# Performance work log

Measured on AMD Instinct MI355X. Metric: run time of the kernel, lower is better.

Reference implementation:

```python
import jax, jax.numpy as jnp
import numpy as np

D = 512      # n_embd
H = 8        # n_head
L = 2        # n_layer (per stack)
T = 2048     # sequence length / block_size
B = 1        # batch
BANDS = (999, 9)  # band_width for [phase, tool] stacks
EPS = 1e-5


def _sinusoidal(n_pos, dim):
    pos = np.arange(n_pos)[:, None].astype(np.float64)
    j = np.arange(dim)[None, :]
    angle = pos / np.power(10000.0, 2 * (j // 2) / dim)
    out = np.zeros((n_pos, dim), np.float32)
    out[:, 0::2] = np.sin(angle[:, 0::2])
    out[:, 1::2] = np.cos(angle[:, 1::2])
    return jnp.asarray(out)


def setup_inputs() -> dict:
    key = jax.random.key(0)
    ks = jax.random.split(key, 8)
    s = 0.02
    rn = lambda k, shp: jax.random.normal(k, shp, jnp.float32) * s
    inp = {
        "x": jax.random.normal(ks[0], (B, T, D), jnp.float32),
        "pos_emb": _sinusoidal(T, D),            # sinusoidal, frozen
        # leading dim 2 = [phase stack, tool stack], then layer dim L
        "ln1_w": jnp.ones((2, L, D)), "ln1_b": jnp.zeros((2, L, D)),
        "ln2_w": jnp.ones((2, L, D)), "ln2_b": jnp.zeros((2, L, D)),
        "Wq": rn(ks[1], (2, L, D, D)), "bq": jnp.zeros((2, L, D)),
        "Wk": rn(ks[2], (2, L, D, D)), "bk": jnp.zeros((2, L, D)),
        "Wv": rn(ks[3], (2, L, D, D)), "bv": jnp.zeros((2, L, D)),
        "Wo": rn(ks[4], (2, L, D, D)), "bo": jnp.zeros((2, L, D)),
        "W1": rn(ks[5], (2, L, D, 2 * D)), "b1": jnp.zeros((2, L, 2 * D)),
        "W2": rn(ks[6], (2, L, 2 * D, D)), "b2": jnp.zeros((2, L, D)),
        "lnf_w": jnp.ones((D,)), "lnf_b": jnp.zeros((D,)),
    }
    return inp


def _ln(x, w, b):
    mu = x.mean(-1, keepdims=True)
    var = ((x - mu) ** 2).mean(-1, keepdims=True)
    return (x - mu) / jnp.sqrt(var + EPS) * w + b


def _attn(x, Wq, bq, Wk, bk, Wv, bv, Wo, bo, bw):
    Bx, Tx, _ = x.shape
    Dh = D // H
    heads = lambda W, b: (x @ W + b).reshape(Bx, Tx, H, Dh).transpose(0, 2, 1, 3)
    q, k, v = heads(Wq, bq), heads(Wk, bk), heads(Wv, bv)
    att = jnp.einsum('bhqd,bhkd->bhqk', q, k) / jnp.sqrt(jnp.float32(Dh))
    i = jnp.arange(Tx)[:, None]
    j = jnp.arange(Tx)[None, :]
    mask = (j <= i) & (j >= i - bw)  # causal band
    att = jnp.where(mask, att, -jnp.inf)
    att = jax.nn.softmax(att, axis=-1)
    y = jnp.einsum('bhqk,bhkd->bhqd', att, v).transpose(0, 2, 1, 3).reshape(Bx, Tx, D)
    return y @ Wo + bo


def reference(x, pos_emb, ln1_w, ln1_b, ln2_w, ln2_b,
              Wq, bq, Wk, bk, Wv, bv, Wo, bo,
              W1, b1, W2, b2, lnf_w, lnf_b):
    Tx = x.shape[1]
    h0 = x + pos_emb[None, :Tx]
    outs = []
    for s in range(2):  # phase stack, tool stack
        bw = BANDS[s]
        h = h0
        for l in range(L):
            h = h + _attn(_ln(h, ln1_w[s, l], ln1_b[s, l]),
                          Wq[s, l], bq[s, l], Wk[s, l], bk[s, l],
                          Wv[s, l], bv[s, l], Wo[s, l], bo[s, l], bw)
            hm = _ln(h, ln2_w[s, l], ln2_b[s, l])
            h = h + (jax.nn.gelu(hm @ W1[s, l] + b1[s, l], approximate=False)
                     @ W2[s, l] + b2[s, l])
        outs.append(_ln(h, lnf_w, lnf_b))
    return (outs[0], outs[1])
```

## Files before the change

kernel.cpp:

```cpp
#include <hip/hip_runtime.h>
#include <stdint.h>

#define T 2048
#define D 512
#define NH 8
#define DH 64
#define L 2

typedef float floatx4 __attribute__((ext_vector_type(4)));
typedef short shortx8 __attribute__((ext_vector_type(8)));
typedef unsigned short u16;
typedef unsigned short u16x4 __attribute__((ext_vector_type(4)));

__device__ __forceinline__ u16 f2bf(float f) {
    union { float f; uint32_t u; } c; c.f = f;
    uint32_t u = c.u;
    u += 0x7fffu + ((u >> 16) & 1u);
    return (u16)(u >> 16);
}

__device__ __forceinline__ float bf2f(u16 v) {
    union { uint32_t u; float f; } c; c.u = ((uint32_t)v) << 16;
    return c.f;
}

__device__ __forceinline__ void load_lds16(const void* g, void* l) {
    __builtin_amdgcn_global_load_lds((const __attribute__((address_space(1))) void*)g,
                                     (__attribute__((address_space(3))) void*)l,
                                     16, 0, 0);
}

struct TransJobs {
    const float* src[6];
    u16* dst[6];
    const float* x;
    const float* pos;
    float* h;
};

__global__ __launch_bounds__(256) void pre_kernel(TransJobs j) {
    __shared__ float tile[32][33];
    int tid = threadIdx.x;
    if (blockIdx.z == 24) {
        int idx = (blockIdx.y * 32 + blockIdx.x) * 256 + tid;
        float4 xv = ((const float4*)j.x)[idx];
        float4 pv = ((const float4*)j.pos)[idx];
        float4 r;
        r.x = xv.x + pv.x; r.y = xv.y + pv.y; r.z = xv.z + pv.z; r.w = xv.w + pv.w;
        ((float4*)j.h)[idx] = r;
        ((float4*)j.h)[idx + (T * D / 4)] = r;
        return;
    }
    int m = blockIdx.z >> 2, slice = blockIdx.z & 3;
    int R = (m == 5) ? 1024 : 512;
    int C = (m == 4) ? 1024 : 512;
    if (blockIdx.x * 32 >= C || blockIdx.y * 32 >= R) return;
    const float* in = j.src[m] + (size_t)slice * R * C;
    u16* out = j.dst[m] + (size_t)slice * R * C;
    int tx = tid & 31, ty = tid >> 5;
    int x = blockIdx.x * 32 + tx;
    int y0 = blockIdx.y * 32;
#pragma unroll
    for (int i = 0; i < 4; i++)
        tile[ty + i * 8][tx] = in[(size_t)(y0 + ty + i * 8) * C + x];
    __syncthreads();
    int ox = y0 + tx;
#pragma unroll
    for (int i = 0; i < 4; i++)
        out[(size_t)(blockIdx.x * 32 + ty + i * 8) * R + ox] = f2bf(tile[tx][ty + i * 8]);
}

__global__ __launch_bounds__(256) void ln_res_kernel(float* __restrict__ h,
                                                     const u16* __restrict__ part,
                                                     const float* __restrict__ w0,
                                                     const float* __restrict__ b0,
                                                     u16* __restrict__ out, int l) {
    int row = blockIdx.x * 4 + (threadIdx.x >> 6);
    int lane = threadIdx.x & 63;
    int s = row >> 11;
    int c0 = lane * 4;
    float* xr = h + (size_t)row * D;
    float4 v0 = *(const float4*)(xr + c0);
    float4 v1 = *(const float4*)(xr + c0 + 256);
    if (part) {
        const u16* p0r = part + (size_t)s * 2 * T * D + (size_t)(row & (T - 1)) * D;
        const u16* p1r = p0r + (size_t)T * D;
        u16x4 a0 = *(const u16x4*)(p0r + c0), a1 = *(const u16x4*)(p0r + c0 + 256);
        u16x4 e0 = *(const u16x4*)(p1r + c0), e1 = *(const u16x4*)(p1r + c0 + 256);
        v0.x += bf2f(a0[0]) + bf2f(e0[0]); v0.y += bf2f(a0[1]) + bf2f(e0[1]);
        v0.z += bf2f(a0[2]) + bf2f(e0[2]); v0.w += bf2f(a0[3]) + bf2f(e0[3]);
        v1.x += bf2f(a1[0]) + bf2f(e1[0]); v1.y += bf2f(a1[1]) + bf2f(e1[1]);
        v1.z += bf2f(a1[2]) + bf2f(e1[2]); v1.w += bf2f(a1[3]) + bf2f(e1[3]);
        *(float4*)(xr + c0) = v0;
        *(float4*)(xr + c0 + 256) = v1;
    }
    float sum = v0.x + v0.y + v0.z + v0.w + v1.x + v1.y + v1.z + v1.w;
    float sq = v0.x*v0.x + v0.y*v0.y + v0.z*v0.z + v0.w*v0.w
             + v1.x*v1.x + v1.y*v1.y + v1.z*v1.z + v1.w*v1.w;
#pragma unroll
    for (int d2 = 1; d2 < 64; d2 <<= 1) { sum += __shfl_xor(sum, d2); sq += __shfl_xor(sq, d2); }
    float mu = sum * (1.0f / D);
    float var = sq * (1.0f / D) - mu * mu;
    float rstd = rsqrtf(var + 1e-5f);
    const float* w = w0 + (size_t)(s * L + l) * D;
    const float* b = b0 + (size_t)(s * L + l) * D;
    u16x4 p0, p1;
#pragma unroll
    for (int jj = 0; jj < 4; jj++) {
        float a = (jj == 0 ? v0.x : jj == 1 ? v0.y : jj == 2 ? v0.z : v0.w);
        p0[jj] = f2bf((a - mu) * rstd * w[c0 + jj] + b[c0 + jj]);
        float c = (jj == 0 ? v1.x : jj == 1 ? v1.y : jj == 2 ? v1.z : v1.w);
        p1[jj] = f2bf((c - mu) * rstd * w[c0 + 256 + jj] + b[c0 + 256 + jj]);
    }
    *(u16x4*)(out + (size_t)row * D + c0) = p0;
    *(u16x4*)(out + (size_t)row * D + c0 + 256) = p1;
}

__global__ __launch_bounds__(256) void lnf_kernel(const float* __restrict__ h,
                                                  const u16* __restrict__ part,
                                                  const float* __restrict__ w,
                                                  const float* __restrict__ b,
                                                  float* __restrict__ out) {
    int row = blockIdx.x * 4 + (threadIdx.x >> 6);
    int lane = threadIdx.x & 63;
    int s = row >> 11;
    int c0 = lane * 4;
    const float* xr = h + (size_t)row * D;
    float4 v0 = *(const float4*)(xr + c0);
    float4 v1 = *(const float4*)(xr + c0 + 256);
    const u16* p0r = part + (size_t)s * 2 * T * D + (size_t)(row & (T - 1)) * D;
    const u16* p1r = p0r + (size_t)T * D;
    u16x4 a0 = *(const u16x4*)(p0r + c0), a1 = *(const u16x4*)(p0r + c0 + 256);
    u16x4 e0 = *(const u16x4*)(p1r + c0), e1 = *(const u16x4*)(p1r + c0 + 256);
    v0.x += bf2f(a0[0]) + bf2f(e0[0]); v0.y += bf2f(a0[1]) + bf2f(e0[1]);
    v0.z += bf2f(a0[2]) + bf2f(e0[2]); v0.w += bf2f(a0[3]) + bf2f(e0[3]);
    v1.x += bf2f(a1[0]) + bf2f(e1[0]); v1.y += bf2f(a1[1]) + bf2f(e1[1]);
    v1.z += bf2f(a1[2]) + bf2f(e1[2]); v1.w += bf2f(a1[3]) + bf2f(e1[3]);
    float sum = v0.x + v0.y + v0.z + v0.w + v1.x + v1.y + v1.z + v1.w;
    float sq = v0.x*v0.x + v0.y*v0.y + v0.z*v0.z + v0.w*v0.w
             + v1.x*v1.x + v1.y*v1.y + v1.z*v1.z + v1.w*v1.w;
#pragma unroll
    for (int d2 = 1; d2 < 64; d2 <<= 1) { sum += __shfl_xor(sum, d2); sq += __shfl_xor(sq, d2); }
    float mu = sum * (1.0f / D);
    float var = sq * (1.0f / D) - mu * mu;
    float rstd = rsqrtf(var + 1e-5f);
    float4 r0, r1;
    r0.x = (v0.x - mu) * rstd * w[c0+0] + b[c0+0];
    r0.y = (v0.y - mu) * rstd * w[c0+1] + b[c0+1];
    r0.z = (v0.z - mu) * rstd * w[c0+2] + b[c0+2];
    r0.w = (v0.w - mu) * rstd * w[c0+3] + b[c0+3];
    r1.x = (v1.x - mu) * rstd * w[c0+256+0] + b[c0+256+0];
    r1.y = (v1.y - mu) * rstd * w[c0+256+1] + b[c0+256+1];
    r1.z = (v1.z - mu) * rstd * w[c0+256+2] + b[c0+256+2];
    r1.w = (v1.w - mu) * rstd * w[c0+256+3] + b[c0+256+3];
    *(float4*)(out + (size_t)row * D + c0) = r0;
    *(float4*)(out + (size_t)row * D + c0 + 256) = r1;
}

struct GemmPtrs {
    const u16* A[6];
    const u16* Bt[6];
    const float* bias[6];
    void* C[6];
};

#define EPI_QKV  0
#define EPI_GELU 1
#define EPI_PART 2

template <int EPI>
__global__ __launch_bounds__(256) void gemm_kernel(GemmPtrs p, int M, int N, int K, int KS) {
    __shared__ __align__(16) u16 lA[2][128 * 32];
    __shared__ __align__(16) u16 lB[2][64 * 32];
    int nchunk = K / KS;
    int pidx = blockIdx.z / nchunk;
    int kc = blockIdx.z % nchunk;
    int koff = kc * KS;
    const u16* A = p.A[pidx];
    const u16* Bt = p.Bt[pidx];
    int m0 = blockIdx.y * 128, n0 = blockIdx.x * 64;
    int tid = threadIdx.x;
    int lane = tid & 63, wave = tid >> 6;
    int wx = wave & 1, wy = wave >> 1;
    int l16 = lane & 15, q4 = lane >> 4;
    const u16* ag = A + (size_t)(m0 + (tid >> 2)) * K + koff + (tid & 3) * 8;
    const u16* bg = Bt + (size_t)(n0 + (tid >> 2)) * K + koff + (tid & 3) * 8;
    size_t rowskip = (size_t)64 * K;
    floatx4 acc[4][2] = {};
    for (int k0 = 0; k0 < KS; k0 += 64) {
        __syncthreads();
#pragma unroll
        for (int kh = 0; kh < 2; kh++) {
            load_lds16(ag + k0 + kh * 32, &lA[kh][tid * 8]);
            load_lds16(ag + rowskip + k0 + kh * 32, &lA[kh][64 * 32 + tid * 8]);
            load_lds16(bg + k0 + kh * 32, &lB[kh][tid * 8]);
        }
        __syncthreads();
#pragma unroll
        for (int kh = 0; kh < 2; kh++) {
            shortx8 af[4], bf[2];
#pragma unroll
            for (int t = 0; t < 4; t++)
                af[t] = *(const shortx8*)(&lA[kh][(wy * 64 + t * 16 + l16) * 32 + q4 * 8]);
#pragma unroll
            for (int t = 0; t < 2; t++)
                bf[t] = *(const shortx8*)(&lB[kh][(wx * 32 + t * 16 + l16) * 32 + q4 * 8]);
#pragma unroll
            for (int i = 0; i < 4; i++)
#pragma unroll
                for (int j = 0; j < 2; j++)
                    acc[i][j] = __builtin_amdgcn_mfma_f32_16x16x32_bf16(af[i], bf[j], acc[i][j], 0, 0, 0);
        }
    }
    const float* bias = p.bias[pidx];
    bool vtrans = (EPI == EPI_QKV) && (pidx % 3 == 2);
#pragma unroll
    for (int i = 0; i < 4; i++) {
        int row0 = m0 + wy * 64 + i * 16 + q4 * 4;
#pragma unroll
        for (int j = 0; j < 2; j++) {
            int col = n0 + wx * 32 + j * 16 + l16;
            float bz = (kc == 0) ? bias[col] : 0.0f;
            floatx4 a = acc[i][j];
            if (EPI == EPI_QKV) {
                if (vtrans) {
                    u16x4 pk;
#pragma unroll
                    for (int r = 0; r < 4; r++) pk[r] = f2bf(a[r] + bz);
                    *(u16x4*)((u16*)p.C[pidx] + (size_t)col * M + row0) = pk;
                } else {
#pragma unroll
                    for (int r = 0; r < 4; r++)
                        ((u16*)p.C[pidx])[(size_t)(row0 + r) * N + col] = f2bf(a[r] + bz);
                }
            } else if (EPI == EPI_GELU) {
#pragma unroll
                for (int r = 0; r < 4; r++) {
                    float v = a[r] + bz;
                    float g = 0.5f * v * (1.0f + erff(v * 0.70710678118f));
                    ((u16*)p.C[pidx])[(size_t)(row0 + r) * N + col] = f2bf(g);
                }
            } else {
#pragma unroll
                for (int r = 0; r < 4; r++)
                    ((u16*)p.C[pidx])[(size_t)kc * M * N + (size_t)(row0 + r) * N + col] = f2bf(a[r] + bz);
            }
        }
    }
}

__global__ __launch_bounds__(256) void attn_kernel(const u16* __restrict__ qg,
                                                   const u16* __restrict__ kg,
                                                   const u16* __restrict__ vtg,
                                                   u16* __restrict__ ao,
                                                   int bw0, int bw1) {
    __shared__ __align__(16) u16 pbuf[4][16 * 32];
    __shared__ float cl[4][16];
    __shared__ float co[4][16][64];
    int s = blockIdx.z, hh = blockIdx.y, q0 = blockIdx.x * 16;
    int bw = (s == 0) ? bw0 : bw1;
    int tid = threadIdx.x, wave = tid >> 6, lane = tid & 63;
    int l16 = lane & 15, q4 = lane >> 4;
    const u16* Q = qg + (size_t)s * T * D;
    const u16* Kp = kg + (size_t)s * T * D;
    const u16* V = vtg + (size_t)s * D * T;
    int hd = hh * DH;
    shortx8 qf0 = *(const shortx8*)(Q + (size_t)(q0 + l16) * D + hd + q4 * 8);
    shortx8 qf1 = *(const shortx8*)(Q + (size_t)(q0 + l16) * D + hd + 32 + q4 * 8);
    floatx4 o[4] = {};
    float lsum[4] = {};
    int klo = q0 - bw; if (klo < 0) klo = 0; klo &= ~31;
    int khi = q0 + 15;
    u16* pw = pbuf[wave];
    for (int kt = klo + wave * 32; kt <= khi; kt += 128) {
        floatx4 s0 = {}, s1 = {};
        {
            shortx8 kf0 = *(const shortx8*)(Kp + (size_t)(kt + l16) * D + hd + q4 * 8);
            shortx8 kf1 = *(const shortx8*)(Kp + (size_t)(kt + l16) * D + hd + 32 + q4 * 8);
            s0 = __builtin_amdgcn_mfma_f32_16x16x32_bf16(qf0, kf0, s0, 0, 0, 0);
            s0 = __builtin_amdgcn_mfma_f32_16x16x32_bf16(qf1, kf1, s0, 0, 0, 0);
            shortx8 kf2 = *(const shortx8*)(Kp + (size_t)(kt + 16 + l16) * D + hd + q4 * 8);
            shortx8 kf3 = *(const shortx8*)(Kp + (size_t)(kt + 16 + l16) * D + hd + 32 + q4 * 8);
            s1 = __builtin_amdgcn_mfma_f32_16x16x32_bf16(qf0, kf2, s1, 0, 0, 0);
            s1 = __builtin_amdgcn_mfma_f32_16x16x32_bf16(qf1, kf3, s1, 0, 0, 0);
        }
#pragma unroll
        for (int r = 0; r < 4; r++) {
            int row = q0 + q4 * 4 + r;
            int c0 = kt + l16, c1 = kt + 16 + l16;
            float p0 = (c0 <= row && c0 >= row - bw) ? __expf(s0[r] * 0.125f) : 0.0f;
            float p1 = (c1 <= row && c1 >= row - bw) ? __expf(s1[r] * 0.125f) : 0.0f;
            float ps = p0 + p1;
#pragma unroll
            for (int d2 = 1; d2 < 16; d2 <<= 1) ps += __shfl_xor(ps, d2);
            lsum[r] += ps;
            pw[(q4 * 4 + r) * 32 + l16] = f2bf(p0);
            pw[(q4 * 4 + r) * 32 + 16 + l16] = f2bf(p1);
        }
        shortx8 pf = *(const shortx8*)(pw + l16 * 32 + q4 * 8);
#pragma unroll
        for (int n = 0; n < 4; n++) {
            shortx8 vf = *(const shortx8*)(V + (size_t)(hd + n * 16 + l16) * T + kt + q4 * 8);
            o[n] = __builtin_amdgcn_mfma_f32_16x16x32_bf16(pf, vf, o[n], 0, 0, 0);
        }
    }
    if (l16 == 0) {
#pragma unroll
        for (int r = 0; r < 4; r++) cl[wave][q4 * 4 + r] = lsum[r];
    }
#pragma unroll
    for (int n = 0; n < 4; n++)
#pragma unroll
        for (int r = 0; r < 4; r++)
            co[wave][q4 * 4 + r][n * 16 + l16] = o[n][r];
    __syncthreads();
#pragma unroll
    for (int i = 0; i < 4; i++) {
        int idx = tid + i * 256;
        int row = idx >> 6, col = idx & 63;
        float Ls = cl[0][row] + cl[1][row] + cl[2][row] + cl[3][row];
        float O = co[0][row][col] + co[1][row][col] + co[2][row][col] + co[3][row][col];
        ao[(size_t)s * T * D + (size_t)(q0 + row) * D + hd + col] = f2bf(O / Ls);
    }
}

extern "C" void kernel_launch(void* const* d_in, const int* in_sizes, int n_in,
                              void* d_out, int out_size, void* d_ws, size_t ws_size,
                              hipStream_t stream) {
    (void)in_sizes; (void)n_in; (void)out_size; (void)ws_size;
    const float* x     = (const float*)d_in[0];
    const float* pos   = (const float*)d_in[1];
    const float* ln1_w = (const float*)d_in[2];
    const float* ln1_b = (const float*)d_in[3];
    const float* ln2_w = (const float*)d_in[4];
    const float* ln2_b = (const float*)d_in[5];
    const float* Wq    = (const float*)d_in[6];
    const float* bq    = (const float*)d_in[7];
    const float* Wk    = (const float*)d_in[8];
    const float* bk    = (const float*)d_in[9];
    const float* Wv    = (const float*)d_in[10];
    const float* bv    = (const float*)d_in[11];
    const float* Wo    = (const float*)d_in[12];
    const float* bo    = (const float*)d_in[13];
    const float* W1    = (const float*)d_in[14];
    const float* b1    = (const float*)d_in[15];
    const float* W2    = (const float*)d_in[16];
    const float* b2    = (const float*)d_in[17];
    const float* lnf_w = (const float*)d_in[18];
    const float* lnf_b = (const float*)d_in[19];

    char* ws = (char*)d_ws;
    size_t off = 0;
    auto alloc = [&](size_t bytes) { void* p = ws + off; off += (bytes + 255) & ~(size_t)255; return p; };
    u16* WqT = (u16*)alloc((size_t)4 * 512 * 512 * 2);
    u16* WkT = (u16*)alloc((size_t)4 * 512 * 512 * 2);
    u16* WvT = (u16*)alloc((size_t)4 * 512 * 512 * 2);
    u16* WoT = (u16*)alloc((size_t)4 * 512 * 512 * 2);
    u16* W1T = (u16*)alloc((size_t)4 * 512 * 1024 * 2);
    u16* W2T = (u16*)alloc((size_t)4 * 1024 * 512 * 2);
    float* h = (float*)alloc((size_t)2 * T * D * 4);
    u16* xln = (u16*)alloc((size_t)2 * T * D * 2);
    u16* qb  = (u16*)alloc((size_t)2 * T * D * 2);
    u16* kb  = (u16*)alloc((size_t)2 * T * D * 2);
    u16* vt  = (u16*)alloc((size_t)2 * T * D * 2);
    u16* ao  = (u16*)alloc((size_t)2 * T * D * 2);
    u16* ff  = (u16*)alloc((size_t)2 * T * 1024 * 2);
    u16* pp = (u16*)alloc((size_t)2 * 2 * T * D * 2);
    u16* pf = (u16*)alloc((size_t)2 * 2 * T * D * 2);

    TransJobs tj;
    tj.src[0] = Wq; tj.dst[0] = WqT;
    tj.src[1] = Wk; tj.dst[1] = WkT;
    tj.src[2] = Wv; tj.dst[2] = WvT;
    tj.src[3] = Wo; tj.dst[3] = WoT;
    tj.src[4] = W1; tj.dst[4] = W1T;
    tj.src[5] = W2; tj.dst[5] = W2T;
    tj.x = x; tj.pos = pos; tj.h = h;
    pre_kernel<<<dim3(32, 32, 25), 256, 0, stream>>>(tj);

    for (int l = 0; l < L; l++) {
        ln_res_kernel<<<(2 * T) / 4, 256, 0, stream>>>(h, l == 0 ? nullptr : pf,
                                                       ln1_w, ln1_b, xln, l);

        GemmPtrs g{};
        for (int s = 0; s < 2; s++) {
            int wo = s * L + l;
            const u16* a = xln + (size_t)s * T * D;
            g.A[s * 3 + 0] = a; g.Bt[s * 3 + 0] = WqT + (size_t)wo * 512 * 512;
            g.bias[s * 3 + 0] = bq + (size_t)wo * 512; g.C[s * 3 + 0] = qb + (size_t)s * T * D;
            g.A[s * 3 + 1] = a; g.Bt[s * 3 + 1] = WkT + (size_t)wo * 512 * 512;
            g.bias[s * 3 + 1] = bk + (size_t)wo * 512; g.C[s * 3 + 1] = kb + (size_t)s * T * D;
            g.A[s * 3 + 2] = a; g.Bt[s * 3 + 2] = WvT + (size_t)wo * 512 * 512;
            g.bias[s * 3 + 2] = bv + (size_t)wo * 512; g.C[s * 3 + 2] = vt + (size_t)s * T * D;
        }
        gemm_kernel<EPI_QKV><<<dim3(8, 16, 6), 256, 0, stream>>>(g, T, 512, 512, 512);

        attn_kernel<<<dim3(128, 8, 2), 256, 0, stream>>>(qb, kb, vt, ao, 999, 9);

        GemmPtrs gp{};
        for (int s = 0; s < 2; s++) {
            int wo = s * L + l;
            gp.A[s] = ao + (size_t)s * T * D;
            gp.Bt[s] = WoT + (size_t)wo * 512 * 512;
            gp.bias[s] = bo + (size_t)wo * 512;
            gp.C[s] = pp + (size_t)s * 2 * T * D;
        }
        gemm_kernel<EPI_PART><<<dim3(8, 16, 4), 256, 0, stream>>>(gp, T, 512, 512, 256);

        ln_res_kernel<<<(2 * T) / 4, 256, 0, stream>>>(h, pp, ln2_w, ln2_b, xln, l);

        GemmPtrs g1{};
        for (int s = 0; s < 2; s++) {
            int wo = s * L + l;
            g1.A[s] = xln + (size_t)s * T * D;
            g1.Bt[s] = W1T + (size_t)wo * 512 * 1024;
            g1.bias[s] = b1 + (size_t)wo * 1024;
            g1.C[s] = ff + (size_t)s * T * 1024;
        }
        gemm_kernel<EPI_GELU><<<dim3(16, 16, 2), 256, 0, stream>>>(g1, T, 1024, 512, 512);

        GemmPtrs g2{};
        for (int s = 0; s < 2; s++) {
            int wo = s * L + l;
            g2.A[s] = ff + (size_t)s * T * 1024;
            g2.Bt[s] = W2T + (size_t)wo * 1024 * 512;
            g2.bias[s] = b2 + (size_t)wo * 512;
            g2.C[s] = pf + (size_t)s * 2 * T * D;
        }
        gemm_kernel<EPI_PART><<<dim3(8, 16, 4), 256, 0, stream>>>(g2, T, 512, 1024, 512);
    }

    lnf_kernel<<<(2 * T) / 4, 256, 0, stream>>>(h, pf, lnf_w, lnf_b, (float*)d_out);
}
```

Measured before the change: 333.2 us.

## Double-buffer GEMM LDS loads and split-K output projections four ways

Result: slower. 355.2 us (+6.6%).

```diff
diff --git a/kernel.cpp b/kernel.cpp
--- a/kernel.cpp
+++ b/kernel.cpp
@@ -83,14 +83,14 @@
     float4 v0 = *(const float4*)(xr + c0);
     float4 v1 = *(const float4*)(xr + c0 + 256);
     if (part) {
-        const u16* p0r = part + (size_t)s * 2 * T * D + (size_t)(row & (T - 1)) * D;
-        const u16* p1r = p0r + (size_t)T * D;
-        u16x4 a0 = *(const u16x4*)(p0r + c0), a1 = *(const u16x4*)(p0r + c0 + 256);
-        u16x4 e0 = *(const u16x4*)(p1r + c0), e1 = *(const u16x4*)(p1r + c0 + 256);
-        v0.x += bf2f(a0[0]) + bf2f(e0[0]); v0.y += bf2f(a0[1]) + bf2f(e0[1]);
-        v0.z += bf2f(a0[2]) + bf2f(e0[2]); v0.w += bf2f(a0[3]) + bf2f(e0[3]);
-        v1.x += bf2f(a1[0]) + bf2f(e1[0]); v1.y += bf2f(a1[1]) + bf2f(e1[1]);
-        v1.z += bf2f(a1[2]) + bf2f(e1[2]); v1.w += bf2f(a1[3]) + bf2f(e1[3]);
+        const u16* pr = part + (size_t)s * 4 * T * D + (size_t)(row & (T - 1)) * D;
+#pragma unroll
+        for (int kc = 0; kc < 4; kc++) {
+            u16x4 a0 = *(const u16x4*)(pr + c0), a1 = *(const u16x4*)(pr + c0 + 256);
+            v0.x += bf2f(a0[0]); v0.y += bf2f(a0[1]); v0.z += bf2f(a0[2]); v0.w += bf2f(a0[3]);
+            v1.x += bf2f(a1[0]); v1.y += bf2f(a1[1]); v1.z += bf2f(a1[2]); v1.w += bf2f(a1[3]);
+            pr += (size_t)T * D;
+        }
         *(float4*)(xr + c0) = v0;
         *(float4*)(xr + c0 + 256) = v1;
     }
@@ -128,14 +128,14 @@
     const float* xr = h + (size_t)row * D;
     float4 v0 = *(const float4*)(xr + c0);
     float4 v1 = *(const float4*)(xr + c0 + 256);
-    const u16* p0r = part + (size_t)s * 2 * T * D + (size_t)(row & (T - 1)) * D;
-    const u16* p1r = p0r + (size_t)T * D;
-    u16x4 a0 = *(const u16x4*)(p0r + c0), a1 = *(const u16x4*)(p0r + c0 + 256);
-    u16x4 e0 = *(const u16x4*)(p1r + c0), e1 = *(const u16x4*)(p1r + c0 + 256);
-    v0.x += bf2f(a0[0]) + bf2f(e0[0]); v0.y += bf2f(a0[1]) + bf2f(e0[1]);
-    v0.z += bf2f(a0[2]) + bf2f(e0[2]); v0.w += bf2f(a0[3]) + bf2f(e0[3]);
-    v1.x += bf2f(a1[0]) + bf2f(e1[0]); v1.y += bf2f(a1[1]) + bf2f(e1[1]);
-    v1.z += bf2f(a1[2]) + bf2f(e1[2]); v1.w += bf2f(a1[3]) + bf2f(e1[3]);
+    const u16* pr = part + (size_t)s * 4 * T * D + (size_t)(row & (T - 1)) * D;
+#pragma unroll
+    for (int kc = 0; kc < 4; kc++) {
+        u16x4 a0 = *(const u16x4*)(pr + c0), a1 = *(const u16x4*)(pr + c0 + 256);
+        v0.x += bf2f(a0[0]); v0.y += bf2f(a0[1]); v0.z += bf2f(a0[2]); v0.w += bf2f(a0[3]);
+        v1.x += bf2f(a1[0]); v1.y += bf2f(a1[1]); v1.z += bf2f(a1[2]); v1.w += bf2f(a1[3]);
+        pr += (size_t)T * D;
+    }
     float sum = v0.x + v0.y + v0.z + v0.w + v1.x + v1.y + v1.z + v1.w;
     float sq = v0.x*v0.x + v0.y*v0.y + v0.z*v0.z + v0.w*v0.w
              + v1.x*v1.x + v1.y*v1.y + v1.z*v1.z + v1.w*v1.w;
@@ -170,8 +170,8 @@
 
 template <int EPI>
 __global__ __launch_bounds__(256) void gemm_kernel(GemmPtrs p, int M, int N, int K, int KS) {
-    __shared__ __align__(16) u16 lA[2][128 * 32];
-    __shared__ __align__(16) u16 lB[2][64 * 32];
+    __shared__ __align__(16) u16 lA[2][128 * 64];
+    __shared__ __align__(16) u16 lB[2][64 * 64];
     int nchunk = K / KS;
     int pidx = blockIdx.z / nchunk;
     int kc = blockIdx.z % nchunk;
@@ -183,34 +183,51 @@
     int lane = tid & 63, wave = tid >> 6;
     int wx = wave & 1, wy = wave >> 1;
     int l16 = lane & 15, q4 = lane >> 4;
-    const u16* ag = A + (size_t)(m0 + (tid >> 2)) * K + koff + (tid & 3) * 8;
-    const u16* bg = Bt + (size_t)(n0 + (tid >> 2)) * K + koff + (tid & 3) * 8;
-    size_t rowskip = (size_t)64 * K;
+    const u16* ag = A + (size_t)(m0 + (tid >> 3)) * K + koff + (tid & 7) * 8;
+    const u16* bg = Bt + (size_t)(n0 + (tid >> 3)) * K + koff + (tid & 7) * 8;
+    size_t rskip32 = (size_t)32 * K;
     floatx4 acc[4][2] = {};
-    for (int k0 = 0; k0 < KS; k0 += 64) {
-        __syncthreads();
-#pragma unroll
-        for (int kh = 0; kh < 2; kh++) {
-            load_lds16(ag + k0 + kh * 32, &lA[kh][tid * 8]);
-            load_lds16(ag + rowskip + k0 + kh * 32, &lA[kh][64 * 32 + tid * 8]);
-            load_lds16(bg + k0 + kh * 32, &lB[kh][tid * 8]);
-        }
-        __syncthreads();
+    int nch = KS / 64;
+    {
+#pragma unroll
+        for (int g = 0; g < 4; g++)
+            load_lds16(ag + g * rskip32, &lA[0][g * (32 * 64) + tid * 8]);
+#pragma unroll
+        for (int g = 0; g < 2; g++)
+            load_lds16(bg + g * rskip32, &lB[0][g * (32 * 64) + tid * 8]);
+    }
+    __syncthreads();
+    for (int c = 0; c < nch; c++) {
+        int b = c & 1;
+        if (c + 1 < nch) {
+            int k0 = (c + 1) * 64;
+#pragma unroll
+            for (int g = 0; g < 4; g++)
+                load_lds16(ag + g * rskip32 + k0, &lA[b ^ 1][g * (32 * 64) + tid * 8]);
+#pragma unroll
+            for (int g = 0; g < 2; g++)
+                load_lds16(bg + g * rskip32 + k0, &lB[b ^ 1][g * (32 * 64) + tid * 8]);
+        }
 #pragma unroll
         for (int kh = 0; kh < 2; kh++) {
             shortx8 af[4], bf[2];
 #pragma unroll
-            for (int t = 0; t < 4; t++)
-                af[t] = *(const shortx8*)(&lA[kh][(wy * 64 + t * 16 + l16) * 32 + q4 * 8]);
-#pragma unroll
-            for (int t = 0; t < 2; t++)
-                bf[t] = *(const shortx8*)(&lB[kh][(wx * 32 + t * 16 + l16) * 32 + q4 * 8]);
+            for (int t = 0; t < 4; t++) {
+                int r = wy * 64 + t * 16 + l16;
+                af[t] = *(const shortx8*)(&lA[b][(r >> 5) * (32 * 64) + (r & 31) * 64 + kh * 32 + q4 * 8]);
+            }
+#pragma unroll
+            for (int t = 0; t < 2; t++) {
+                int r = wx * 32 + t * 16 + l16;
+                bf[t] = *(const shortx8*)(&lB[b][(r >> 5) * (32 * 64) + (r & 31) * 64 + kh * 32 + q4 * 8]);
+            }
 #pragma unroll
             for (int i = 0; i < 4; i++)
 #pragma unroll
                 for (int j = 0; j < 2; j++)
                     acc[i][j] = __builtin_amdgcn_mfma_f32_16x16x32_bf16(af[i], bf[j], acc[i][j], 0, 0, 0);
         }
+        __syncthreads();
     }
     const float* bias = p.bias[pidx];
     bool vtrans = (EPI == EPI_QKV) && (pidx % 3 == 2);
@@ -365,8 +382,8 @@
     u16* vt  = (u16*)alloc((size_t)2 * T * D * 2);
     u16* ao  = (u16*)alloc((size_t)2 * T * D * 2);
     u16* ff  = (u16*)alloc((size_t)2 * T * 1024 * 2);
-    u16* pp = (u16*)alloc((size_t)2 * 2 * T * D * 2);
-    u16* pf = (u16*)alloc((size_t)2 * 2 * T * D * 2);
+    u16* pp = (u16*)alloc((size_t)2 * 4 * T * D * 2);
+    u16* pf = (u16*)alloc((size_t)2 * 4 * T * D * 2);
 
     TransJobs tj;
     tj.src[0] = Wq; tj.dst[0] = WqT;
@@ -403,9 +420,9 @@
             gp.A[s] = ao + (size_t)s * T * D;
             gp.Bt[s] = WoT + (size_t)wo * 512 * 512;
             gp.bias[s] = bo + (size_t)wo * 512;
-            gp.C[s] = pp + (size_t)s * 2 * T * D;
-        }
-        gemm_kernel<EPI_PART><<<dim3(8, 16, 4), 256, 0, stream>>>(gp, T, 512, 512, 256);
+            gp.C[s] = pp + (size_t)s * 4 * T * D;
+        }
+        gemm_kernel<EPI_PART><<<dim3(8, 16, 8), 256, 0, stream>>>(gp, T, 512, 512, 128);
 
         ln_res_kernel<<<(2 * T) / 4, 256, 0, stream>>>(h, pp, ln2_w, ln2_b, xln, l);
 
@@ -425,9 +442,9 @@
             g2.A[s] = ff + (size_t)s * T * 1024;
             g2.Bt[s] = W2T + (size_t)wo * 1024 * 512;
             g2.bias[s] = b2 + (size_t)wo * 512;
-            g2.C[s] = pf + (size_t)s * 2 * T * D;
-        }
-        gemm_kernel<EPI_PART><<<dim3(8, 16, 4), 256, 0, stream>>>(g2, T, 512, 1024, 512);
+            g2.C[s] = pf + (size_t)s * 4 * T * D;
+        }
+        gemm_kernel<EPI_PART><<<dim3(8, 16, 8), 256, 0, stream>>>(g2, T, 512, 1024, 256);
     }
 
     lnf_kernel<<<(2 * T) / 4, 256, 0, stream>>>(h, pf, lnf_w, lnf_b, (float*)d_out);
```
